# Performance work log

Measured on AMD Instinct MI355X. Metric: run time of the kernel, lower is better.

## Reference

```python
import jax, jax.numpy as jnp
import numpy as np

N = 50000
E = 1600000
F_IN = 3
C = 40

def _linear_params(key, fan_in, fan_out):
    k1, k2 = jax.random.split(key)
    bound = 1.0 / np.sqrt(fan_in)
    W = jax.random.uniform(k1, (fan_in, fan_out), jnp.float32, -bound, bound)
    b = jax.random.uniform(k2, (fan_out,), jnp.float32, -bound, bound)
    return W, b

def setup_inputs() -> dict:
    key = jax.random.key(0)
    ks = jax.random.split(key, 9)
    x = jax.random.normal(ks[0], (N, F_IN), jnp.float32)
    pos = jax.random.normal(ks[1], (N, 3), jnp.float32)
    edge_index = jax.random.randint(ks[2], (2, E), 0, N, jnp.int64)
    W1, b1 = _linear_params(ks[3], F_IN + 3, 64)   # local_nn layer 1
    W2, b2 = _linear_params(ks[4], 64, 64)          # local_nn layer 2
    W3, b3 = _linear_params(ks[5], 64, 128)         # global_nn layer 1
    W4, b4 = _linear_params(ks[6], 128, 1024)       # global_nn layer 2
    W5, b5 = _linear_params(ks[7], 1024, 64)        # global_nn layer 3
    Wf, bf = _linear_params(ks[8], 64, C)           # fc
    return {"x": x, "pos": pos, "edge_index": edge_index,
            "W1": W1, "b1": b1, "W2": W2, "b2": b2,
            "W3": W3, "b3": b3, "W4": W4, "b4": b4,
            "W5": W5, "b5": b5, "Wf": Wf, "bf": bf}

def reference(x, pos, edge_index, W1, b1, W2, b2, W3, b3, W4, b4, W5, b5, Wf, bf):
    # PyG PointNetConv: add self-loops by default
    loop = jnp.arange(N, dtype=edge_index.dtype)
    src = jnp.concatenate([edge_index[0], loop])  # j
    dst = jnp.concatenate([edge_index[1], loop])  # i
    # message: local_nn(concat(x_j, pos_j - pos_i))  -> [E+N, 64]
    msg_in = jnp.concatenate([x[src], pos[src] - pos[dst]], axis=1)
    h = jax.nn.relu(msg_in @ W1 + b1)
    h = h @ W2 + b2
    # max-aggregate to destination nodes
    agg = jax.ops.segment_max(h, dst, num_segments=N)
    # global_nn
    g = jax.nn.relu(agg @ W3 + b3)
    g = jax.nn.relu(g @ W4 + b4)
    g = g @ W5 + b5
    # trailing relu + fc + log_softmax
    out = jax.nn.relu(g) @ Wf + bf
    return jax.nn.log_softmax(out, axis=1)
```

## Files before the change

### kernel.cpp

```cpp
#include <hip/hip_runtime.h>
#include <cstddef>
#include <cmath>

typedef __attribute__((ext_vector_type(8))) short bf16x8;
typedef __attribute__((ext_vector_type(4))) float f32x4;

static __device__ __forceinline__ f32x4 mfma16(bf16x8 a, bf16x8 b, f32x4 c) {
    return __builtin_amdgcn_mfma_f32_16x16x32_bf16(a, b, c, 0, 0, 0);
}
static __device__ __forceinline__ unsigned short f2bf(float f) {
    unsigned int u = __float_as_uint(f);
    return (unsigned short)((u + 0x7FFFu + ((u >> 16) & 1u)) >> 16);
}

#define NBK 256
#define CAP 12288

__global__ __launch_bounds__(256) void k_bin_conv(
    const int* __restrict__ ei, int E,
    unsigned int* __restrict__ gcur, unsigned int* __restrict__ pairs, int binBlocks,
    const float* __restrict__ W1, const float* __restrict__ W2,
    const float* __restrict__ W3, const float* __restrict__ W4,
    const float* __restrict__ W5,
    unsigned short* __restrict__ W1bt, unsigned short* __restrict__ W2bt,
    unsigned short* __restrict__ W3bt, unsigned short* __restrict__ W4bt,
    unsigned short* __restrict__ W5ct)
{
    int tid = threadIdx.x;
    if (blockIdx.x >= binBlocks) {
        int id = (blockIdx.x - binBlocks) * 256 + tid;
        if (id < 2048) {
            int n = id >> 5, k = id & 31;
            W1bt[id] = (k < 6) ? f2bf(W1[k * 64 + n]) : (unsigned short)0;
        } else if (id < 2048 + 4096) {
            int t = id - 2048;
            int n = t >> 6, k = t & 63;
            W2bt[t] = f2bf(W2[k * 64 + n]);
        } else if (id < 6144 + 8192) {
            int t = id - 6144;
            int n = t >> 6, k = t & 63;
            W3bt[t] = f2bf(W3[k * 128 + n]);
        } else if (id < 14336 + 131072) {
            int t = id - 14336;
            int n = t >> 7, k = t & 127;
            W4bt[t] = f2bf(W4[k * 1024 + n]);
        } else if (id < 145408 + 65536) {
            int t = id - 145408;
            int ch = t >> 12, rem = t & 4095;
            int n = rem >> 6, kl = rem & 63;
            W5ct[t] = f2bf(W5[(ch * 64 + kl) * 64 + n]);
        }
        return;
    }
    __shared__ unsigned int h[NBK];
    __shared__ unsigned int base[NBK];
    h[tid] = 0u;
    __syncthreads();
    int idx = blockIdx.x * 256 + tid;
    int e0 = idx * 4;
    unsigned int vals[4]; int bs[4]; unsigned int rk[4]; int cnt4 = 0;
    if (e0 + 3 < E) {
        int4 s = ((const int4*)ei)[idx];
        int4 d = ((const int4*)(ei + E))[idx];
        int sa[4] = {s.x, s.y, s.z, s.w};
        int da[4] = {d.x, d.y, d.z, d.w};
        cnt4 = 4;
#pragma unroll
        for (int j = 0; j < 4; ++j) {
            bs[j] = da[j] >> 8;
            vals[j] = (unsigned int)sa[j] | ((unsigned int)(da[j] & 255) << 16);
            rk[j] = atomicAdd(&h[bs[j]], 1u);
        }
    } else {
        for (int e = e0; e < E; ++e) {
            int j = cnt4++;
            int sv = ei[e], dv = ei[E + e];
            bs[j] = dv >> 8;
            vals[j] = (unsigned int)sv | ((unsigned int)(dv & 255) << 16);
            rk[j] = atomicAdd(&h[bs[j]], 1u);
        }
    }
    __syncthreads();
    unsigned int c = h[tid];
    base[tid] = c ? atomicAdd(&gcur[tid], c) : 0u;
    __syncthreads();
    for (int j = 0; j < cnt4; ++j) {
        unsigned int p = base[bs[j]] + rk[j];
        if (p < CAP) pairs[(size_t)bs[j] * CAP + p] = vals[j];
    }
}

__global__ __launch_bounds__(256) void k_build(const unsigned int* __restrict__ gcur,
                                               const unsigned int* __restrict__ pairs,
                                               unsigned int* __restrict__ list,
                                               unsigned int* __restrict__ off,
                                               unsigned int* __restrict__ deg, int N) {
    __shared__ unsigned int cntL[NBK];
    __shared__ unsigned int s[NBK];
    __shared__ unsigned int curL[NBK];
    int b = blockIdx.x, t = threadIdx.x;
    unsigned int gstart = (unsigned int)b * CAP;
    unsigned int m = min(gcur[b], (unsigned int)CAP);
    cntL[t] = 0u;
    __syncthreads();
    for (unsigned int i = t; i < m; i += 256u)
        atomicAdd(&cntL[(pairs[gstart + i] >> 16) & 255u], 1u);
    __syncthreads();
    unsigned int c = cntL[t];
    s[t] = c;
    __syncthreads();
    for (int d = 1; d < 256; d <<= 1) {
        unsigned int v = (t >= d) ? s[t - d] : 0u;
        __syncthreads();
        s[t] += v;
        __syncthreads();
    }
    unsigned int excl = s[t] - c;
    int dst = b * 256 + t;
    if (dst < N) { off[dst] = gstart + excl; deg[dst] = c; }
    curL[t] = excl;
    __syncthreads();
    for (unsigned int i = t; i < m; i += 256u) {
        unsigned int v = pairs[gstart + i];
        unsigned int p = atomicAdd(&curL[(v >> 16) & 255u], 1u);
        list[gstart + p] = v & 0xFFFFu;
    }
}

#define TPB_E 256
#define EDGE_WPB 4
__global__ __launch_bounds__(TPB_E, 4) void edge_kernel(
    const float* __restrict__ x, const float* __restrict__ pos,
    const unsigned int* __restrict__ off, const unsigned int* __restrict__ deg,
    const unsigned int* __restrict__ list,
    const unsigned short* __restrict__ W1bt, const float* __restrict__ b1,
    const unsigned short* __restrict__ W2bt, const float* __restrict__ b2,
    float* __restrict__ agg, int N, int dstStride)
{
    __shared__ __align__(16) short Hs[4][16 * 72];

    int tid = threadIdx.x;
    int lane = tid & 63;
    int w = tid >> 6;
    int lm = lane & 15;
    int quad = lane >> 4;
    short* H = Hs[w];
    int dst0 = blockIdx.x * EDGE_WPB + w;

    bf16x8 B1f[4], B2f[4][2];
    float4 b1v[4];
    float b2c[4];
#pragma unroll
    for (int nt = 0; nt < 4; ++nt) {
        B1f[nt] = *(const bf16x8*)&W1bt[(nt * 16 + lm) * 32 + quad * 8];
        B2f[nt][0] = *(const bf16x8*)&W2bt[(nt * 16 + lm) * 64 + quad * 8];
        B2f[nt][1] = *(const bf16x8*)&W2bt[(nt * 16 + lm) * 64 + 32 + quad * 8];
        b1v[nt] = *(const float4*)&b1[nt * 16 + quad * 4];
        b2c[nt] = b2[nt * 16 + lm];
    }

    unsigned int o0P = 0u, dgP = 0u;
    if (dst0 < N) { o0P = off[dst0]; dgP = deg[dst0]; }

    for (int dst = dst0; dst < N; dst += dstStride) {
        unsigned int o0 = o0P;
        int ecnt = (int)dgP;
        int dn = dst + dstStride;
        if (dn < N) { o0P = off[dn]; dgP = deg[dn]; }

        int M = ecnt + 1;
        float pi0 = pos[dst * 3 + 0], pi1 = pos[dst * 3 + 1], pi2 = pos[dst * 3 + 2];

        float m0 = -INFINITY, m1 = -INFINITY, m2 = -INFINITY, m3 = -INFINITY;

        auto ldidx = [&](int base) -> int {
            int i = min(base + lm, M - 1);
            return (i == 0) ? dst : (int)list[o0 + i - 1];
        };

        float vx0 = 0.f, vx1 = 0.f, vx2 = 0.f, vq0 = 0.f, vq1 = 0.f, vq2 = 0.f;
        int sNext = dst;
        if (quad == 0) {
            int s0 = ldidx(0);
            vx0 = x[s0 * 3 + 0]; vx1 = x[s0 * 3 + 1]; vx2 = x[s0 * 3 + 2];
            vq0 = pos[s0 * 3 + 0]; vq1 = pos[s0 * 3 + 1]; vq2 = pos[s0 * 3 + 2];
            if (16 < M) sNext = ldidx(16);
        }

        for (int base = 0; base < M; base += 16) {
            float nx0 = vx0, nx1 = vx1, nx2 = vx2, nq0 = vq0, nq1 = vq1, nq2 = vq2;
            int sN2 = sNext;
            if (quad == 0) {
                nx0 = x[sNext * 3 + 0]; nx1 = x[sNext * 3 + 1]; nx2 = x[sNext * 3 + 2];
                nq0 = pos[sNext * 3 + 0]; nq1 = pos[sNext * 3 + 1]; nq2 = pos[sNext * 3 + 2];
                if (base + 32 < M) sN2 = ldidx(base + 32);
            }
            bf16x8 A = {0, 0, 0, 0, 0, 0, 0, 0};
            if (quad == 0) {
                A[0] = (short)f2bf(vx0);
                A[1] = (short)f2bf(vx1);
                A[2] = (short)f2bf(vx2);
                A[3] = (short)f2bf(vq0 - pi0);
                A[4] = (short)f2bf(vq1 - pi1);
                A[5] = (short)f2bf(vq2 - pi2);
            }
#pragma unroll
            for (int nt = 0; nt < 4; ++nt) {
                f32x4 c = {0.f, 0.f, 0.f, 0.f};
                c = mfma16(B1f[nt], A, c);
                float4 bb = b1v[nt];
                unsigned int u0 = (unsigned int)f2bf(fmaxf(c[0] + bb.x, 0.f)) |
                                  ((unsigned int)f2bf(fmaxf(c[1] + bb.y, 0.f)) << 16);
                unsigned int u1 = (unsigned int)f2bf(fmaxf(c[2] + bb.z, 0.f)) |
                                  ((unsigned int)f2bf(fmaxf(c[3] + bb.w, 0.f)) << 16);
                *(uint2*)&H[lm * 72 + nt * 16 + quad * 4] = make_uint2(u0, u1);
            }
            bf16x8 A2a = *(const bf16x8*)&H[lm * 72 + quad * 8];
            bf16x8 A2b = *(const bf16x8*)&H[lm * 72 + 32 + quad * 8];
            {
                f32x4 c = {0.f, 0.f, 0.f, 0.f};
                c = mfma16(A2a, B2f[0][0], c); c = mfma16(A2b, B2f[0][1], c);
                m0 = fmaxf(m0, fmaxf(fmaxf(c[0], c[1]), fmaxf(c[2], c[3])));
            }
            {
                f32x4 c = {0.f, 0.f, 0.f, 0.f};
                c = mfma16(A2a, B2f[1][0], c); c = mfma16(A2b, B2f[1][1], c);
                m1 = fmaxf(m1, fmaxf(fmaxf(c[0], c[1]), fmaxf(c[2], c[3])));
            }
            {
                f32x4 c = {0.f, 0.f, 0.f, 0.f};
                c = mfma16(A2a, B2f[2][0], c); c = mfma16(A2b, B2f[2][1], c);
                m2 = fmaxf(m2, fmaxf(fmaxf(c[0], c[1]), fmaxf(c[2], c[3])));
            }
            {
                f32x4 c = {0.f, 0.f, 0.f, 0.f};
                c = mfma16(A2a, B2f[3][0], c); c = mfma16(A2b, B2f[3][1], c);
                m3 = fmaxf(m3, fmaxf(fmaxf(c[0], c[1]), fmaxf(c[2], c[3])));
            }
            vx0 = nx0; vx1 = nx1; vx2 = nx2; vq0 = nq0; vq1 = nq1; vq2 = nq2;
            sNext = sN2;
        }

        m0 = fmaxf(m0, __shfl_xor(m0, 16, 64)); m0 = fmaxf(m0, __shfl_xor(m0, 32, 64));
        m1 = fmaxf(m1, __shfl_xor(m1, 16, 64)); m1 = fmaxf(m1, __shfl_xor(m1, 32, 64));
        m2 = fmaxf(m2, __shfl_xor(m2, 16, 64)); m2 = fmaxf(m2, __shfl_xor(m2, 32, 64));
        m3 = fmaxf(m3, __shfl_xor(m3, 16, 64)); m3 = fmaxf(m3, __shfl_xor(m3, 32, 64));

        float mv = (quad == 0) ? m0 : (quad == 1) ? m1 : (quad == 2) ? m2 : m3;
        agg[(size_t)dst * 64 + lane] = mv + b2c[quad];
    }
}

#define NNODE 64
__global__ __launch_bounds__(512, 4) void node_kernel(
    const float* __restrict__ agg,
    const unsigned short* __restrict__ W3bt, const float* __restrict__ b3,
    const unsigned short* __restrict__ W4bt, const float* __restrict__ b4,
    const unsigned short* __restrict__ W5ct, const float* __restrict__ b5,
    const float* __restrict__ Wf, const float* __restrict__ bf,
    float* __restrict__ out, int N)
{
    __shared__ __align__(16) char smem[79872];
    short* G1s = (short*)smem;
    float* G3f = (float*)smem;
    short* G2s = (short*)(smem + 17408);
    short* Wb4 = (short*)(smem + 26624);
    short* Wb5 = (short*)(smem + 61440);
    float* os  = (float*)(smem + 26624);

    int tid = threadIdx.x;
    int lane = tid & 63;
    int wm = tid >> 6;
    int m = wm & 3;
    int h = wm >> 2;
    int lm = lane & 15;
    int quad = lane >> 4;
    int n0 = blockIdx.x * NNODE;

    int4 s4a, s4b, s5;
    auto stage_load = [&](int ch) {
        const unsigned short* g4 = W4bt + (size_t)ch * 8192;
        s4a = *(const int4*)(g4 + tid * 8);
        s4b = *(const int4*)(g4 + (tid + 512) * 8);
        s5  = *(const int4*)(W5ct + (size_t)ch * 4096 + tid * 8);
    };
    auto stage_store = [&](int buf) {
        short* d4 = Wb4 + buf * 8704;
        *(int4*)&d4[(tid >> 4) * 136 + (tid & 15) * 8] = s4a;
        int v1 = tid + 512;
        *(int4*)&d4[(v1 >> 4) * 136 + (v1 & 15) * 8] = s4b;
        short* d5 = Wb5 + buf * 4608;
        *(int4*)&d5[(tid >> 3) * 72 + (tid & 7) * 8] = s5;
    };

    stage_load(0);
    stage_store(0);

    {
        int arow = min(n0 + m * 16 + lm, N - 1);
        bf16x8 A3[2];
#pragma unroll
        for (int f = 0; f < 2; ++f) {
            const float* p = agg + (size_t)arow * 64 + f * 32 + quad * 8;
            float4 u = *(const float4*)p;
            float4 v = *(const float4*)(p + 4);
            bf16x8 t;
            t[0] = (short)f2bf(u.x); t[1] = (short)f2bf(u.y);
            t[2] = (short)f2bf(u.z); t[3] = (short)f2bf(u.w);
            t[4] = (short)f2bf(v.x); t[5] = (short)f2bf(v.y);
            t[6] = (short)f2bf(v.z); t[7] = (short)f2bf(v.w);
            A3[f] = t;
        }
#pragma unroll
        for (int nt2 = 0; nt2 < 4; ++nt2) {
            int nt = h * 4 + nt2;
            const unsigned short* wb = W3bt + (nt * 16 + lm) * 64 + quad * 8;
            f32x4 c = {0.f, 0.f, 0.f, 0.f};
            c = mfma16(*(const bf16x8*)wb, A3[0], c);
            c = mfma16(*(const bf16x8*)(wb + 32), A3[1], c);
            float4 bb = *(const float4*)&b3[nt * 16 + quad * 4];
            unsigned int u0 = (unsigned int)f2bf(fmaxf(c[0] + bb.x, 0.f)) |
                              ((unsigned int)f2bf(fmaxf(c[1] + bb.y, 0.f)) << 16);
            unsigned int u1 = (unsigned int)f2bf(fmaxf(c[2] + bb.z, 0.f)) |
                              ((unsigned int)f2bf(fmaxf(c[3] + bb.w, 0.f)) << 16);
            *(uint2*)&G1s[(m * 16 + lm) * 136 + nt * 16 + quad * 4] = make_uint2(u0, u1);
        }
    }

    f32x4 acc3[4];
#pragma unroll
    for (int nt = 0; nt < 4; ++nt) {
        float b = (h == 0) ? b5[nt * 16 + lm] : 0.f;
        acc3[nt][0] = b; acc3[nt][1] = b; acc3[nt][2] = b; acc3[nt][3] = b;
    }

    __syncthreads();

    bf16x8 A4[4];
#pragma unroll
    for (int f = 0; f < 4; ++f)
        A4[f] = *(const bf16x8*)&G1s[(m * 16 + lm) * 136 + f * 32 + quad * 8];

    for (int ch = 0; ch < 16; ++ch) {
        int buf = ch & 1;
        if (ch < 15) stage_load(ch + 1);
        __builtin_amdgcn_sched_barrier(0);

        const short* w4b = Wb4 + buf * 8704;
        const short* w5b = Wb5 + buf * 4608;

#pragma unroll
        for (int nt2 = 0; nt2 < 2; ++nt2) {
            int nt = h * 2 + nt2;
            const short* wb = w4b + (nt * 16 + lm) * 136 + quad * 8;
            f32x4 c = {0.f, 0.f, 0.f, 0.f};
            c = mfma16(*(const bf16x8*)wb, A4[0], c);
            c = mfma16(*(const bf16x8*)(wb + 32), A4[1], c);
            c = mfma16(*(const bf16x8*)(wb + 64), A4[2], c);
            c = mfma16(*(const bf16x8*)(wb + 96), A4[3], c);
            float4 bb = *(const float4*)&b4[ch * 64 + nt * 16 + quad * 4];
            unsigned int u0 = (unsigned int)f2bf(fmaxf(c[0] + bb.x, 0.f)) |
                              ((unsigned int)f2bf(fmaxf(c[1] + bb.y, 0.f)) << 16);
            unsigned int u1 = (unsigned int)f2bf(fmaxf(c[2] + bb.z, 0.f)) |
                              ((unsigned int)f2bf(fmaxf(c[3] + bb.w, 0.f)) << 16);
            *(uint2*)&G2s[(m * 16 + lm) * 72 + nt * 16 + quad * 4] = make_uint2(u0, u1);
        }
        bf16x8 A5 = *(const bf16x8*)&G2s[(m * 16 + lm) * 72 + h * 32 + quad * 8];
#pragma unroll
        for (int nt = 0; nt < 4; ++nt) {
            const short* wb = w5b + (nt * 16 + lm) * 72 + h * 32 + quad * 8;
            acc3[nt] = mfma16(A5, *(const bf16x8*)wb, acc3[nt]);
        }
        if (ch < 15) stage_store(buf ^ 1);
        __syncthreads();
    }

    if (h == 0) {
#pragma unroll
        for (int nt = 0; nt < 4; ++nt)
#pragma unroll
            for (int r = 0; r < 4; ++r)
                G3f[(m * 16 + quad * 4 + r) * 68 + nt * 16 + lm] = acc3[nt][r];
    }
    __syncthreads();
    if (h == 1) {
#pragma unroll
        for (int nt = 0; nt < 4; ++nt)
#pragma unroll
            for (int r = 0; r < 4; ++r) {
                int idx = (m * 16 + quad * 4 + r) * 68 + nt * 16 + lm;
                G3f[idx] = fmaxf(G3f[idx] + acc3[nt][r], 0.f);
            }
    }
    __syncthreads();

    for (int idx = tid; idx < NNODE * 40; idx += 512) {
        int ln = idx / 40;
        int c = idx - ln * 40;
        float o = bf[c];
#pragma unroll 4
        for (int j = 0; j < 64; ++j)
            o = fmaf(G3f[ln * 68 + j], Wf[j * 40 + c], o);
        os[ln * 41 + c] = o;
    }
    __syncthreads();

    if (tid < NNODE && n0 + tid < N) {
        int ln = tid;
        float mx = os[ln * 41 + 0];
#pragma unroll
        for (int c = 1; c < 40; ++c) mx = fmaxf(mx, os[ln * 41 + c]);
        float s = 0.f;
#pragma unroll
        for (int c = 0; c < 40; ++c) s += expf(os[ln * 41 + c] - mx);
        float ls = logf(s) + mx;
        float* op = out + (size_t)(n0 + tid) * 40;
#pragma unroll
        for (int c = 0; c < 40; ++c) op[c] = os[ln * 41 + c] - ls;
    }
}

extern "C" void kernel_launch(void* const* d_in, const int* in_sizes, int n_in,
                              void* d_out, int out_size, void* d_ws, size_t ws_size,
                              hipStream_t stream) {
    const float* x   = (const float*)d_in[0];
    const float* pos = (const float*)d_in[1];
    const int*   ei  = (const int*)d_in[2];
    const float* W1  = (const float*)d_in[3];
    const float* b1  = (const float*)d_in[4];
    const float* W2  = (const float*)d_in[5];
    const float* b2  = (const float*)d_in[6];
    const float* W3  = (const float*)d_in[7];
    const float* b3  = (const float*)d_in[8];
    const float* W4  = (const float*)d_in[9];
    const float* b4  = (const float*)d_in[10];
    const float* W5  = (const float*)d_in[11];
    const float* b5  = (const float*)d_in[12];
    const float* Wf  = (const float*)d_in[13];
    const float* bf  = (const float*)d_in[14];
    float* out = (float*)d_out;

    int Nn = in_sizes[0] / 3;
    int E  = in_sizes[2] / 2;

    char* w = (char*)d_ws;
    size_t p = 0;
    auto take = [&](size_t bytes) { size_t q = p; p = (p + bytes + 255) & ~size_t(255); return (void*)(w + q); };
    unsigned int*   off   = (unsigned int*)take((size_t)Nn * 4);
    unsigned int*   deg   = (unsigned int*)take((size_t)Nn * 4);
    unsigned int*   gcur  = (unsigned int*)take(NBK * 4);
    unsigned int*   list  = (unsigned int*)take((size_t)NBK * CAP * 4);
    float*          agg   = (float*)take((size_t)Nn * 64 * 4);
    unsigned int*   pairs = (unsigned int*)agg;
    unsigned short* W1bt = (unsigned short*)take(2048 * 2);
    unsigned short* W2bt = (unsigned short*)take(4096 * 2);
    unsigned short* W3bt = (unsigned short*)take(8192 * 2);
    unsigned short* W4bt = (unsigned short*)take(131072 * 2);
    unsigned short* W5ct = (unsigned short*)take(65536 * 2);

    hipMemsetAsync(gcur, 0, NBK * 4, stream);
    int q4 = (E + 3) / 4;
    int gb = (q4 + 255) / 256;
    int cb = (2048 + 4096 + 8192 + 131072 + 65536) / 256;
    k_bin_conv<<<gb + cb, 256, 0, stream>>>(ei, E, gcur, pairs, gb,
                                            W1, W2, W3, W4, W5,
                                            W1bt, W2bt, W3bt, W4bt, W5ct);
    int nb = (Nn + 255) >> 8;
    k_build<<<nb, 256, 0, stream>>>(gcur, pairs, list, off, deg, Nn);

    int totalWaves = (Nn + 3) / 4;
    int eBlocks = (totalWaves + EDGE_WPB - 1) / EDGE_WPB;
    int dstStride = eBlocks * EDGE_WPB;
    edge_kernel<<<eBlocks, TPB_E, 0, stream>>>(
        x, pos, off, deg, list, W1bt, b1, W2bt, b2, agg, Nn, dstStride);

    node_kernel<<<(Nn + NNODE - 1) / NNODE, 512, 0, stream>>>(
        agg, W3bt, b3, W4bt, b4, W5ct, b5, Wf, bf, out, Nn);
}
```

Measured before the change: 301.8 us.

## Fuse edge message/max-aggregation kernel into node MLP kernel via shared memory

Merges the edge kernel into the node kernel. Each 512-thread block first computes the max-aggregated 64-wide features for its 64 destination nodes (8 per wave) into shared memory, then runs the global MLP on them. This removes the global agg buffer round trip and one kernel launch. The cost is that the edge phase now runs at the node kernel's occupancy and block shape, and it drops the software prefetch of neighbour indices and features. The pairs buffer gets its own workspace allocation instead of aliasing agg.

```diff
diff --git a/kernel.cpp b/kernel.cpp
--- a/kernel.cpp
+++ b/kernel.cpp
@@ -127,133 +127,13 @@
     }
 }
 
-#define TPB_E 256
-#define EDGE_WPB 4
-__global__ __launch_bounds__(TPB_E, 4) void edge_kernel(
+#define NNODE 64
+__global__ __launch_bounds__(512, 4) void fused_kernel(
     const float* __restrict__ x, const float* __restrict__ pos,
     const unsigned int* __restrict__ off, const unsigned int* __restrict__ deg,
     const unsigned int* __restrict__ list,
     const unsigned short* __restrict__ W1bt, const float* __restrict__ b1,
     const unsigned short* __restrict__ W2bt, const float* __restrict__ b2,
-    float* __restrict__ agg, int N, int dstStride)
-{
-    __shared__ __align__(16) short Hs[4][16 * 72];
-
-    int tid = threadIdx.x;
-    int lane = tid & 63;
-    int w = tid >> 6;
-    int lm = lane & 15;
-    int quad = lane >> 4;
-    short* H = Hs[w];
-    int dst0 = blockIdx.x * EDGE_WPB + w;
-
-    bf16x8 B1f[4], B2f[4][2];
-    float4 b1v[4];
-    float b2c[4];
-#pragma unroll
-    for (int nt = 0; nt < 4; ++nt) {
-        B1f[nt] = *(const bf16x8*)&W1bt[(nt * 16 + lm) * 32 + quad * 8];
-        B2f[nt][0] = *(const bf16x8*)&W2bt[(nt * 16 + lm) * 64 + quad * 8];
-        B2f[nt][1] = *(const bf16x8*)&W2bt[(nt * 16 + lm) * 64 + 32 + quad * 8];
-        b1v[nt] = *(const float4*)&b1[nt * 16 + quad * 4];
-        b2c[nt] = b2[nt * 16 + lm];
-    }
-
-    unsigned int o0P = 0u, dgP = 0u;
-    if (dst0 < N) { o0P = off[dst0]; dgP = deg[dst0]; }
-
-    for (int dst = dst0; dst < N; dst += dstStride) {
-        unsigned int o0 = o0P;
-        int ecnt = (int)dgP;
-        int dn = dst + dstStride;
-        if (dn < N) { o0P = off[dn]; dgP = deg[dn]; }
-
-        int M = ecnt + 1;
-        float pi0 = pos[dst * 3 + 0], pi1 = pos[dst * 3 + 1], pi2 = pos[dst * 3 + 2];
-
-        float m0 = -INFINITY, m1 = -INFINITY, m2 = -INFINITY, m3 = -INFINITY;
-
-        auto ldidx = [&](int base) -> int {
-            int i = min(base + lm, M - 1);
-            return (i == 0) ? dst : (int)list[o0 + i - 1];
-        };
-
-        float vx0 = 0.f, vx1 = 0.f, vx2 = 0.f, vq0 = 0.f, vq1 = 0.f, vq2 = 0.f;
-        int sNext = dst;
-        if (quad == 0) {
-            int s0 = ldidx(0);
-            vx0 = x[s0 * 3 + 0]; vx1 = x[s0 * 3 + 1]; vx2 = x[s0 * 3 + 2];
-            vq0 = pos[s0 * 3 + 0]; vq1 = pos[s0 * 3 + 1]; vq2 = pos[s0 * 3 + 2];
-            if (16 < M) sNext = ldidx(16);
-        }
-
-        for (int base = 0; base < M; base += 16) {
-            float nx0 = vx0, nx1 = vx1, nx2 = vx2, nq0 = vq0, nq1 = vq1, nq2 = vq2;
-            int sN2 = sNext;
-            if (quad == 0) {
-                nx0 = x[sNext * 3 + 0]; nx1 = x[sNext * 3 + 1]; nx2 = x[sNext * 3 + 2];
-                nq0 = pos[sNext * 3 + 0]; nq1 = pos[sNext * 3 + 1]; nq2 = pos[sNext * 3 + 2];
-                if (base + 32 < M) sN2 = ldidx(base + 32);
-            }
-            bf16x8 A = {0, 0, 0, 0, 0, 0, 0, 0};
-            if (quad == 0) {
-                A[0] = (short)f2bf(vx0);
-                A[1] = (short)f2bf(vx1);
-                A[2] = (short)f2bf(vx2);
-                A[3] = (short)f2bf(vq0 - pi0);
-                A[4] = (short)f2bf(vq1 - pi1);
-                A[5] = (short)f2bf(vq2 - pi2);
-            }
-#pragma unroll
-            for (int nt = 0; nt < 4; ++nt) {
-                f32x4 c = {0.f, 0.f, 0.f, 0.f};
-                c = mfma16(B1f[nt], A, c);
-                float4 bb = b1v[nt];
-                unsigned int u0 = (unsigned int)f2bf(fmaxf(c[0] + bb.x, 0.f)) |
-                                  ((unsigned int)f2bf(fmaxf(c[1] + bb.y, 0.f)) << 16);
-                unsigned int u1 = (unsigned int)f2bf(fmaxf(c[2] + bb.z, 0.f)) |
-                                  ((unsigned int)f2bf(fmaxf(c[3] + bb.w, 0.f)) << 16);
-                *(uint2*)&H[lm * 72 + nt * 16 + quad * 4] = make_uint2(u0, u1);
-            }
-            bf16x8 A2a = *(const bf16x8*)&H[lm * 72 + quad * 8];
-            bf16x8 A2b = *(const bf16x8*)&H[lm * 72 + 32 + quad * 8];
-            {
-                f32x4 c = {0.f, 0.f, 0.f, 0.f};
-                c = mfma16(A2a, B2f[0][0], c); c = mfma16(A2b, B2f[0][1], c);
-                m0 = fmaxf(m0, fmaxf(fmaxf(c[0], c[1]), fmaxf(c[2], c[3])));
-            }
-            {
-                f32x4 c = {0.f, 0.f, 0.f, 0.f};
-                c = mfma16(A2a, B2f[1][0], c); c = mfma16(A2b, B2f[1][1], c);
-                m1 = fmaxf(m1, fmaxf(fmaxf(c[0], c[1]), fmaxf(c[2], c[3])));
-            }
-            {
-                f32x4 c = {0.f, 0.f, 0.f, 0.f};
-                c = mfma16(A2a, B2f[2][0], c); c = mfma16(A2b, B2f[2][1], c);
-                m2 = fmaxf(m2, fmaxf(fmaxf(c[0], c[1]), fmaxf(c[2], c[3])));
-            }
-            {
-                f32x4 c = {0.f, 0.f, 0.f, 0.f};
-                c = mfma16(A2a, B2f[3][0], c); c = mfma16(A2b, B2f[3][1], c);
-                m3 = fmaxf(m3, fmaxf(fmaxf(c[0], c[1]), fmaxf(c[2], c[3])));
-            }
-            vx0 = nx0; vx1 = nx1; vx2 = nx2; vq0 = nq0; vq1 = nq1; vq2 = nq2;
-            sNext = sN2;
-        }
-
-        m0 = fmaxf(m0, __shfl_xor(m0, 16, 64)); m0 = fmaxf(m0, __shfl_xor(m0, 32, 64));
-        m1 = fmaxf(m1, __shfl_xor(m1, 16, 64)); m1 = fmaxf(m1, __shfl_xor(m1, 32, 64));
-        m2 = fmaxf(m2, __shfl_xor(m2, 16, 64)); m2 = fmaxf(m2, __shfl_xor(m2, 32, 64));
-        m3 = fmaxf(m3, __shfl_xor(m3, 16, 64)); m3 = fmaxf(m3, __shfl_xor(m3, 32, 64));
-
-        float mv = (quad == 0) ? m0 : (quad == 1) ? m1 : (quad == 2) ? m2 : m3;
-        agg[(size_t)dst * 64 + lane] = mv + b2c[quad];
-    }
-}
-
-#define NNODE 64
-__global__ __launch_bounds__(512, 4) void node_kernel(
-    const float* __restrict__ agg,
     const unsigned short* __restrict__ W3bt, const float* __restrict__ b3,
     const unsigned short* __restrict__ W4bt, const float* __restrict__ b4,
     const unsigned short* __restrict__ W5ct, const float* __restrict__ b5,
@@ -261,21 +141,106 @@
     float* __restrict__ out, int N)
 {
     __shared__ __align__(16) char smem[79872];
-    short* G1s = (short*)smem;
-    float* G3f = (float*)smem;
-    short* G2s = (short*)(smem + 17408);
-    short* Wb4 = (short*)(smem + 26624);
-    short* Wb5 = (short*)(smem + 61440);
-    float* os  = (float*)(smem + 26624);
+    float* aggL = (float*)smem;
+    short* G1s  = (short*)smem;
+    float* G3f  = (float*)smem;
+    short* G2s  = (short*)(smem + 17408);
+    short* Wb4  = (short*)(smem + 26624);
+    short* HsB  = (short*)(smem + 26624);
+    short* Wb5  = (short*)(smem + 61440);
+    float* os   = (float*)(smem + 26624);
 
     int tid = threadIdx.x;
     int lane = tid & 63;
     int wm = tid >> 6;
-    int m = wm & 3;
-    int h = wm >> 2;
     int lm = lane & 15;
     int quad = lane >> 4;
     int n0 = blockIdx.x * NNODE;
+
+    {
+        short* H = HsB + wm * 1152;
+        bf16x8 B1f[4], B2f[4][2];
+        float4 b1v[4];
+        float b2c[4];
+#pragma unroll
+        for (int nt = 0; nt < 4; ++nt) {
+            B1f[nt] = *(const bf16x8*)&W1bt[(nt * 16 + lm) * 32 + quad * 8];
+            B2f[nt][0] = *(const bf16x8*)&W2bt[(nt * 16 + lm) * 64 + quad * 8];
+            B2f[nt][1] = *(const bf16x8*)&W2bt[(nt * 16 + lm) * 64 + 32 + quad * 8];
+            b1v[nt] = *(const float4*)&b1[nt * 16 + quad * 4];
+            b2c[nt] = b2[nt * 16 + lm];
+        }
+
+        for (int it = 0; it < 8; ++it) {
+            int row = wm * 8 + it;
+            int dst = n0 + row;
+            if (dst >= N) { aggL[row * 68 + lane] = 0.f; continue; }
+
+            unsigned int o0 = off[dst];
+            int M = (int)deg[dst] + 1;
+            float pi0 = pos[dst * 3 + 0], pi1 = pos[dst * 3 + 1], pi2 = pos[dst * 3 + 2];
+
+            float m0 = -INFINITY, m1 = -INFINITY, m2 = -INFINITY, m3 = -INFINITY;
+
+            for (int base = 0; base < M; base += 16) {
+                bf16x8 A = {0, 0, 0, 0, 0, 0, 0, 0};
+                if (quad == 0) {
+                    int i = min(base + lm, M - 1);
+                    int s = (i == 0) ? dst : (int)list[o0 + i - 1];
+                    A[0] = (short)f2bf(x[s * 3 + 0]);
+                    A[1] = (short)f2bf(x[s * 3 + 1]);
+                    A[2] = (short)f2bf(x[s * 3 + 2]);
+                    A[3] = (short)f2bf(pos[s * 3 + 0] - pi0);
+                    A[4] = (short)f2bf(pos[s * 3 + 1] - pi1);
+                    A[5] = (short)f2bf(pos[s * 3 + 2] - pi2);
+                }
+#pragma unroll
+                for (int nt = 0; nt < 4; ++nt) {
+                    f32x4 c = {0.f, 0.f, 0.f, 0.f};
+                    c = mfma16(B1f[nt], A, c);
+                    float4 bb = b1v[nt];
+                    unsigned int u0 = (unsigned int)f2bf(fmaxf(c[0] + bb.x, 0.f)) |
+                                      ((unsigned int)f2bf(fmaxf(c[1] + bb.y, 0.f)) << 16);
+                    unsigned int u1 = (unsigned int)f2bf(fmaxf(c[2] + bb.z, 0.f)) |
+                                      ((unsigned int)f2bf(fmaxf(c[3] + bb.w, 0.f)) << 16);
+                    *(uint2*)&H[lm * 72 + nt * 16 + quad * 4] = make_uint2(u0, u1);
+                }
+                bf16x8 A2a = *(const bf16x8*)&H[lm * 72 + quad * 8];
+                bf16x8 A2b = *(const bf16x8*)&H[lm * 72 + 32 + quad * 8];
+                {
+                    f32x4 c = {0.f, 0.f, 0.f, 0.f};
+                    c = mfma16(A2a, B2f[0][0], c); c = mfma16(A2b, B2f[0][1], c);
+                    m0 = fmaxf(m0, fmaxf(fmaxf(c[0], c[1]), fmaxf(c[2], c[3])));
+                }
+                {
+                    f32x4 c = {0.f, 0.f, 0.f, 0.f};
+                    c = mfma16(A2a, B2f[1][0], c); c = mfma16(A2b, B2f[1][1], c);
+                    m1 = fmaxf(m1, fmaxf(fmaxf(c[0], c[1]), fmaxf(c[2], c[3])));
+                }
+                {
+                    f32x4 c = {0.f, 0.f, 0.f, 0.f};
+                    c = mfma16(A2a, B2f[2][0], c); c = mfma16(A2b, B2f[2][1], c);
+                    m2 = fmaxf(m2, fmaxf(fmaxf(c[0], c[1]), fmaxf(c[2], c[3])));
+                }
+                {
+                    f32x4 c = {0.f, 0.f, 0.f, 0.f};
+                    c = mfma16(A2a, B2f[3][0], c); c = mfma16(A2b, B2f[3][1], c);
+                    m3 = fmaxf(m3, fmaxf(fmaxf(c[0], c[1]), fmaxf(c[2], c[3])));
+                }
+            }
+
+            m0 = fmaxf(m0, __shfl_xor(m0, 16, 64)); m0 = fmaxf(m0, __shfl_xor(m0, 32, 64));
+            m1 = fmaxf(m1, __shfl_xor(m1, 16, 64)); m1 = fmaxf(m1, __shfl_xor(m1, 32, 64));
+            m2 = fmaxf(m2, __shfl_xor(m2, 16, 64)); m2 = fmaxf(m2, __shfl_xor(m2, 32, 64));
+            m3 = fmaxf(m3, __shfl_xor(m3, 16, 64)); m3 = fmaxf(m3, __shfl_xor(m3, 32, 64));
+
+            float mv = (quad == 0) ? m0 : (quad == 1) ? m1 : (quad == 2) ? m2 : m3;
+            aggL[row * 68 + lane] = mv + b2c[quad];
+        }
+    }
+
+    int m = wm & 3;
+    int h = wm >> 2;
 
     int4 s4a, s4b, s5;
     auto stage_load = [&](int ch) {
@@ -294,37 +259,37 @@
     };
 
     stage_load(0);
+    __syncthreads();
     stage_store(0);
 
-    {
-        int arow = min(n0 + m * 16 + lm, N - 1);
-        bf16x8 A3[2];
-#pragma unroll
-        for (int f = 0; f < 2; ++f) {
-            const float* p = agg + (size_t)arow * 64 + f * 32 + quad * 8;
-            float4 u = *(const float4*)p;
-            float4 v = *(const float4*)(p + 4);
-            bf16x8 t;
-            t[0] = (short)f2bf(u.x); t[1] = (short)f2bf(u.y);
-            t[2] = (short)f2bf(u.z); t[3] = (short)f2bf(u.w);
-            t[4] = (short)f2bf(v.x); t[5] = (short)f2bf(v.y);
-            t[6] = (short)f2bf(v.z); t[7] = (short)f2bf(v.w);
-            A3[f] = t;
-        }
-#pragma unroll
-        for (int nt2 = 0; nt2 < 4; ++nt2) {
-            int nt = h * 4 + nt2;
-            const unsigned short* wb = W3bt + (nt * 16 + lm) * 64 + quad * 8;
-            f32x4 c = {0.f, 0.f, 0.f, 0.f};
-            c = mfma16(*(const bf16x8*)wb, A3[0], c);
-            c = mfma16(*(const bf16x8*)(wb + 32), A3[1], c);
-            float4 bb = *(const float4*)&b3[nt * 16 + quad * 4];
-            unsigned int u0 = (unsigned int)f2bf(fmaxf(c[0] + bb.x, 0.f)) |
-                              ((unsigned int)f2bf(fmaxf(c[1] + bb.y, 0.f)) << 16);
-            unsigned int u1 = (unsigned int)f2bf(fmaxf(c[2] + bb.z, 0.f)) |
-                              ((unsigned int)f2bf(fmaxf(c[3] + bb.w, 0.f)) << 16);
-            *(uint2*)&G1s[(m * 16 + lm) * 136 + nt * 16 + quad * 4] = make_uint2(u0, u1);
-        }
+    bf16x8 A3[2];
+#pragma unroll
+    for (int f = 0; f < 2; ++f) {
+        const float* p = aggL + (m * 16 + lm) * 68 + f * 32 + quad * 8;
+        float4 u = *(const float4*)p;
+        float4 v = *(const float4*)(p + 4);
+        bf16x8 t;
+        t[0] = (short)f2bf(u.x); t[1] = (short)f2bf(u.y);
+        t[2] = (short)f2bf(u.z); t[3] = (short)f2bf(u.w);
+        t[4] = (short)f2bf(v.x); t[5] = (short)f2bf(v.y);
+        t[6] = (short)f2bf(v.z); t[7] = (short)f2bf(v.w);
+        A3[f] = t;
+    }
+    __syncthreads();
+
+#pragma unroll
+    for (int nt2 = 0; nt2 < 4; ++nt2) {
+        int nt = h * 4 + nt2;
+        const unsigned short* wb = W3bt + (nt * 16 + lm) * 64 + quad * 8;
+        f32x4 c = {0.f, 0.f, 0.f, 0.f};
+        c = mfma16(*(const bf16x8*)wb, A3[0], c);
+        c = mfma16(*(const bf16x8*)(wb + 32), A3[1], c);
+        float4 bb = *(const float4*)&b3[nt * 16 + quad * 4];
+        unsigned int u0 = (unsigned int)f2bf(fmaxf(c[0] + bb.x, 0.f)) |
+                          ((unsigned int)f2bf(fmaxf(c[1] + bb.y, 0.f)) << 16);
+        unsigned int u1 = (unsigned int)f2bf(fmaxf(c[2] + bb.z, 0.f)) |
+                          ((unsigned int)f2bf(fmaxf(c[3] + bb.w, 0.f)) << 16);
+        *(uint2*)&G1s[(m * 16 + lm) * 136 + nt * 16 + quad * 4] = make_uint2(u0, u1);
     }
 
     f32x4 acc3[4];
@@ -450,8 +415,7 @@
     unsigned int*   deg   = (unsigned int*)take((size_t)Nn * 4);
     unsigned int*   gcur  = (unsigned int*)take(NBK * 4);
     unsigned int*   list  = (unsigned int*)take((size_t)NBK * CAP * 4);
-    float*          agg   = (float*)take((size_t)Nn * 64 * 4);
-    unsigned int*   pairs = (unsigned int*)agg;
+    unsigned int*   pairs = (unsigned int*)take((size_t)NBK * CAP * 4);
     unsigned short* W1bt = (unsigned short*)take(2048 * 2);
     unsigned short* W2bt = (unsigned short*)take(4096 * 2);
     unsigned short* W3bt = (unsigned short*)take(8192 * 2);
@@ -468,12 +432,7 @@
     int nb = (Nn + 255) >> 8;
     k_build<<<nb, 256, 0, stream>>>(gcur, pairs, list, off, deg, Nn);
 
-    int totalWaves = (Nn + 3) / 4;
-    int eBlocks = (totalWaves + EDGE_WPB - 1) / EDGE_WPB;
-    int dstStride = eBlocks * EDGE_WPB;
-    edge_kernel<<<eBlocks, TPB_E, 0, stream>>>(
-        x, pos, off, deg, list, W1bt, b1, W2bt, b2, agg, Nn, dstStride);
-
-    node_kernel<<<(Nn + NNODE - 1) / NNODE, 512, 0, stream>>>(
-        agg, W3bt, b3, W4bt, b4, W5ct, b5, Wf, bf, out, Nn);
-}
+    fused_kernel<<<(Nn + NNODE - 1) / NNODE, 512, 0, stream>>>(
+        x, pos, off, deg, list, W1bt, b1, W2bt, b2,
+        W3bt, b3, W4bt, b4, W5ct, b5, Wf, bf, out, Nn);
+}
```

Result: no change. 301.4 us (-0.2%).
